# Kernel tuning notes

Measured on AMD Instinct MI355X. Metric: run time of the kernel, lower is better.

The kernel has to match this reference:

```python
import jax, jax.numpy as jnp
import numpy as np

NUM_CLASSES = 1000
BATCH = 32768
MAX_M = 0.5
S = 30.0


def setup_inputs() -> dict:
    key = jax.random.key(0)
    k1, k2 = jax.random.split(key)
    logits = jax.random.normal(k1, (BATCH, NUM_CLASSES), dtype=jnp.float32)
    # Long-tailed class counts: exponential decay from 100000 to 20 over 1000 classes
    counts = np.exp(np.linspace(np.log(100000.0), np.log(20.0), NUM_CLASSES)).astype(np.float32)
    margins = jnp.asarray(MAX_M / counts ** 0.25)  # [C]
    targets = jax.random.randint(k2, (BATCH,), 0, NUM_CLASSES, dtype=jnp.int64)
    return {"logits": logits, "margins": margins, "targets": targets}


def reference(logits, margins, targets):
    # Subtract the per-class margin only at each sample's target position
    # (vectorized form of the original per-sample scatter loop).
    rows = jnp.arange(logits.shape[0])
    adjusted = logits.at[rows, targets].add(-margins[targets])  # [B, C]
    scaled = S * adjusted
    logp = jax.nn.log_softmax(scaled, axis=-1)  # [B, C]
    nll = -logp[rows, targets]  # [B]
    return jnp.mean(nll)
```

## Files before the change

kernel.cpp:

```cpp
#include <hip/hip_runtime.h>
#include <math.h>

#define BATCH 32768
#define NCLS  1000
#define NVEC  250
#define SCALE 30.0f
#define K_LOG2E 43.28085122666891f
#define LN2 0.69314718055994531f
#define NBLOCKS (BATCH / 4)

__global__ __launch_bounds__(256) void ldam_kernel(
    const float* __restrict__ logits,
    const float* __restrict__ margins,
    const int*   __restrict__ targets,
    float*       __restrict__ partials)
{
    const int wave = threadIdx.x >> 6;
    const int lane = threadIdx.x & 63;
    const int row  = blockIdx.x * 4 + wave;

    const int   t  = targets[row];
    const float mt = margins[t];
    const float4* rowv = (const float4*)(logits + (size_t)row * NCLS);

    float s[16];
    float st = -INFINITY;
    #pragma unroll
    for (int j = 0; j < 4; ++j) {
        const int idx = lane + 64 * j;
        float4 v;
        if (idx < NVEC) {
            v = rowv[idx];
            const int base = 4 * idx;
            if (base + 0 == t) { v.x -= mt; st = v.x; }
            if (base + 1 == t) { v.y -= mt; st = v.y; }
            if (base + 2 == t) { v.z -= mt; st = v.z; }
            if (base + 3 == t) { v.w -= mt; st = v.w; }
        } else {
            v = make_float4(-INFINITY, -INFINITY, -INFINITY, -INFINITY);
        }
        s[4*j + 0] = v.x;
        s[4*j + 1] = v.y;
        s[4*j + 2] = v.z;
        s[4*j + 3] = v.w;
    }

    float m = s[0];
    #pragma unroll
    for (int k = 1; k < 16; ++k) m = fmaxf(m, s[k]);
    #pragma unroll
    for (int off = 1; off < 64; off <<= 1) {
        m  = fmaxf(m,  __shfl_xor(m,  off));
        st = fmaxf(st, __shfl_xor(st, off));
    }

    float l = 0.0f;
    #pragma unroll
    for (int k = 0; k < 16; ++k)
        l += __builtin_amdgcn_exp2f(K_LOG2E * (s[k] - m));
    #pragma unroll
    for (int off = 1; off < 64; off <<= 1)
        l += __shfl_xor(l, off);

    const float nll = SCALE * (m - st) + LN2 * __builtin_amdgcn_logf(l);

    __shared__ float partial[4];
    if (lane == 0) partial[wave] = nll;
    __syncthreads();
    if (threadIdx.x == 0) {
        partials[blockIdx.x] = partial[0] + partial[1] + partial[2] + partial[3];
    }
}

__global__ __launch_bounds__(256) void ldam_reduce_kernel(
    const float* __restrict__ partials,
    float*       __restrict__ out)
{
    const int tid  = threadIdx.x;
    const int lane = tid & 63;
    const int wave = tid >> 6;

    const float4* pv = (const float4*)partials;
    float sum = 0.0f;
    #pragma unroll
    for (int j = 0; j < 8; ++j) {
        const float4 v = pv[tid + 256 * j];
        sum += (v.x + v.y) + (v.z + v.w);
    }

    #pragma unroll
    for (int off = 1; off < 64; off <<= 1)
        sum += __shfl_xor(sum, off);

    __shared__ float ws[4];
    if (lane == 0) ws[wave] = sum;
    __syncthreads();
    if (tid == 0) {
        const float total = ws[0] + ws[1] + ws[2] + ws[3];
        out[0] = total * (1.0f / (float)BATCH);
    }
}

extern "C" void kernel_launch(void* const* d_in, const int* in_sizes, int n_in,
                              void* d_out, int out_size, void* d_ws, size_t ws_size,
                              hipStream_t stream) {
    const float* logits  = (const float*)d_in[0];
    const float* margins = (const float*)d_in[1];
    const int*   targets = (const int*)d_in[2];
    float* out      = (float*)d_out;
    float* partials = (float*)d_ws;

    ldam_kernel<<<NBLOCKS, 256, 0, stream>>>(logits, margins, targets, partials);
    ldam_reduce_kernel<<<1, 256, 0, stream>>>(partials, out);
}
```

Baseline: 189.2 us.

## Process four rows per wave with software-prefetched next-row loads

Each wave now handles four consecutive rows instead of one. It loads the targets as an int4 and prefetches the next row's logits into registers while computing the current row's log-softmax. This cuts the block count by four and shrinks the partials reduction to match. The aim is to hide global load latency within a wave and reduce per-block overhead. The cost is higher register pressure and fewer waves available to hide latency through occupancy.

```diff
diff --git a/kernel.cpp b/kernel.cpp
--- a/kernel.cpp
+++ b/kernel.cpp
@@ -7,7 +7,51 @@
 #define SCALE 30.0f
 #define K_LOG2E 43.28085122666891f
 #define LN2 0.69314718055994531f
-#define NBLOCKS (BATCH / 4)
+#define RPW 4
+#define NBLOCKS (BATCH / (4 * RPW))
+
+__device__ __forceinline__ void load_row(const float4* __restrict__ rowv, int lane,
+                                         float4 w[4]) {
+    w[0] = rowv[lane];
+    w[1] = rowv[lane + 64];
+    w[2] = rowv[lane + 128];
+    if (lane < NVEC - 192)
+        w[3] = rowv[lane + 192];
+    else
+        w[3] = make_float4(-INFINITY, -INFINITY, -INFINITY, -INFINITY);
+}
+
+__device__ __forceinline__ float row_nll(const float4 w[4], int lane, int t, float mt) {
+    float s[16];
+    float st = -INFINITY;
+    #pragma unroll
+    for (int j = 0; j < 4; ++j) {
+        float4 v = w[j];
+        const int base = 4 * (lane + 64 * j);
+        if (base + 0 == t) { v.x -= mt; st = v.x; }
+        if (base + 1 == t) { v.y -= mt; st = v.y; }
+        if (base + 2 == t) { v.z -= mt; st = v.z; }
+        if (base + 3 == t) { v.w -= mt; st = v.w; }
+        s[4*j + 0] = v.x; s[4*j + 1] = v.y;
+        s[4*j + 2] = v.z; s[4*j + 3] = v.w;
+    }
+    float m = s[0];
+    #pragma unroll
+    for (int k = 1; k < 16; ++k) m = fmaxf(m, s[k]);
+    #pragma unroll
+    for (int off = 1; off < 64; off <<= 1) {
+        m  = fmaxf(m,  __shfl_xor(m,  off));
+        st = fmaxf(st, __shfl_xor(st, off));
+    }
+    float l = 0.0f;
+    #pragma unroll
+    for (int k = 0; k < 16; ++k)
+        l += __builtin_amdgcn_exp2f(K_LOG2E * (s[k] - m));
+    #pragma unroll
+    for (int off = 1; off < 64; off <<= 1)
+        l += __shfl_xor(l, off);
+    return SCALE * (m - st) + LN2 * __builtin_amdgcn_logf(l);
+}
 
 __global__ __launch_bounds__(256) void ldam_kernel(
     const float* __restrict__ logits,
@@ -17,59 +61,33 @@
 {
     const int wave = threadIdx.x >> 6;
     const int lane = threadIdx.x & 63;
-    const int row  = blockIdx.x * 4 + wave;
+    const int wid  = blockIdx.x * 4 + wave;
+    const int row0 = wid * RPW;
 
-    const int   t  = targets[row];
-    const float mt = margins[t];
-    const float4* rowv = (const float4*)(logits + (size_t)row * NCLS);
+    const int4 tv = *(const int4*)(targets + row0);
+    const int   ts[4]  = {tv.x, tv.y, tv.z, tv.w};
+    const float mts[4] = {margins[tv.x], margins[tv.y], margins[tv.z], margins[tv.w]};
 
-    float s[16];
-    float st = -INFINITY;
+    const float4* rowv = (const float4*)(logits + (size_t)row0 * NCLS);
+
+    float4 cur[4], nxt[4];
+    load_row(rowv, lane, cur);
+
+    float acc = 0.0f;
     #pragma unroll
-    for (int j = 0; j < 4; ++j) {
-        const int idx = lane + 64 * j;
-        float4 v;
-        if (idx < NVEC) {
-            v = rowv[idx];
-            const int base = 4 * idx;
-            if (base + 0 == t) { v.x -= mt; st = v.x; }
-            if (base + 1 == t) { v.y -= mt; st = v.y; }
-            if (base + 2 == t) { v.z -= mt; st = v.z; }
-            if (base + 3 == t) { v.w -= mt; st = v.w; }
-        } else {
-            v = make_float4(-INFINITY, -INFINITY, -INFINITY, -INFINITY);
-        }
-        s[4*j + 0] = v.x;
-        s[4*j + 1] = v.y;
-        s[4*j + 2] = v.z;
-        s[4*j + 3] = v.w;
+    for (int r = 0; r < RPW; ++r) {
+        if (r + 1 < RPW)
+            load_row(rowv + (size_t)(r + 1) * NVEC, lane, nxt);
+        acc += row_nll(cur, lane, ts[r], mts[r]);
+        #pragma unroll
+        for (int j = 0; j < 4; ++j) cur[j] = nxt[j];
     }
 
-    float m = s[0];
-    #pragma unroll
-    for (int k = 1; k < 16; ++k) m = fmaxf(m, s[k]);
-    #pragma unroll
-    for (int off = 1; off < 64; off <<= 1) {
-        m  = fmaxf(m,  __shfl_xor(m,  off));
-        st = fmaxf(st, __shfl_xor(st, off));
-    }
-
-    float l = 0.0f;
-    #pragma unroll
-    for (int k = 0; k < 16; ++k)
-        l += __builtin_amdgcn_exp2f(K_LOG2E * (s[k] - m));
-    #pragma unroll
-    for (int off = 1; off < 64; off <<= 1)
-        l += __shfl_xor(l, off);
-
-    const float nll = SCALE * (m - st) + LN2 * __builtin_amdgcn_logf(l);
-
-    __shared__ float partial[4];
-    if (lane == 0) partial[wave] = nll;
+    __shared__ float part[4];
+    if (lane == 0) part[wave] = acc;
     __syncthreads();
-    if (threadIdx.x == 0) {
-        partials[blockIdx.x] = partial[0] + partial[1] + partial[2] + partial[3];
-    }
+    if (threadIdx.x == 0)
+        partials[blockIdx.x] = part[0] + part[1] + part[2] + part[3];
 }
 
 __global__ __launch_bounds__(256) void ldam_reduce_kernel(
@@ -83,7 +101,7 @@
     const float4* pv = (const float4*)partials;
     float sum = 0.0f;
     #pragma unroll
-    for (int j = 0; j < 8; ++j) {
+    for (int j = 0; j < 2; ++j) {
         const float4 v = pv[tid + 256 * j];
         sum += (v.x + v.y) + (v.z + v.w);
     }
@@ -92,13 +110,11 @@
     for (int off = 1; off < 64; off <<= 1)
         sum += __shfl_xor(sum, off);
 
-    __shared__ float ws[4];
-    if (lane == 0) ws[wave] = sum;
+    __shared__ float ws_[4];
+    if (lane == 0) ws_[wave] = sum;
     __syncthreads();
-    if (tid == 0) {
-        const float total = ws[0] + ws[1] + ws[2] + ws[3];
-        out[0] = total * (1.0f / (float)BATCH);
-    }
+    if (tid == 0)
+        out[0] = (ws_[0] + ws_[1] + ws_[2] + ws_[3]) * (1.0f / (float)BATCH);
 }
 
 extern "C" void kernel_launch(void* const* d_in, const int* in_sizes, int n_in,
```

New measurement: 189.9 us. No clear change (+0.4%).
